# Kernel tuning notes

Hardware: AMD Instinct MI355X
Metric: run time of the kernel (lower is better)

The kernel has to match this reference:

```python
import jax, jax.numpy as jnp
import numpy as np
import math

B, S, D, H = 4, 1024, 1024, 16
HD = D // H  # 64
EPS = 1e-6
LOG2E = 1.442695041


def setup_inputs() -> dict:
    key = jax.random.key(0)
    ks = jax.random.split(key, 8)
    inputs_q = jax.random.normal(ks[0], (B, S, D), dtype=jnp.float32)
    patch_mask = jnp.zeros((B, S), dtype=bool)
    w_scale = 0.02
    Wq = jax.random.normal(ks[1], (D, D), dtype=jnp.float32) * w_scale
    Wk = jax.random.normal(ks[2], (D, D), dtype=jnp.float32) * w_scale
    Wv = jax.random.normal(ks[3], (D, D), dtype=jnp.float32) * w_scale
    Wo = jax.random.normal(ks[4], (D, D), dtype=jnp.float32) * w_scale
    # RMSNorm scales (torch inits to zero; use random nonzero for a meaningful baseline)
    q_ln_scale = jax.random.uniform(ks[5], (HD,), dtype=jnp.float32, minval=0.5, maxval=1.5)
    k_ln_scale = jax.random.uniform(ks[6], (HD,), dtype=jnp.float32, minval=0.5, maxval=1.5)
    per_dim_scale = jax.random.normal(ks[7], (HD,), dtype=jnp.float32) * 0.1
    return {"inputs_q": inputs_q, "patch_mask": patch_mask, "Wq": Wq, "Wk": Wk,
            "Wv": Wv, "Wo": Wo, "q_ln_scale": q_ln_scale, "k_ln_scale": k_ln_scale,
            "per_dim_scale": per_dim_scale}


def _rope(x, position):
    # x: [b, s, h, hd]; position: [b, s] (float)
    half = HD // 2
    fraction = 2.0 * jnp.arange(half, dtype=x.dtype) / HD
    timescale = 10000.0 ** fraction  # min_timescale=1, max=10000
    sinusoid = position[:, :, None, None] / timescale[None, None, None, :]
    sin, cos = jnp.sin(sinusoid), jnp.cos(sinusoid)
    x1, x2 = jnp.split(x, 2, axis=-1)
    return jnp.concatenate([x1 * cos - x2 * sin, x2 * cos + x1 * sin], axis=-1)


def _rms_norm(x, scale):
    var = jnp.mean(jnp.square(x), axis=-1, keepdims=True)
    return x * jax.lax.rsqrt(var + EPS) * scale


def reference(inputs_q, patch_mask, Wq, Wk, Wv, Wo, q_ln_scale, k_ln_scale, per_dim_scale):
    b, n, _ = inputs_q.shape
    # torch nn.Linear: y = x @ W.T
    q = jnp.einsum('bsd,fd->bsf', inputs_q, Wq).reshape(b, n, H, HD)
    k = jnp.einsum('bsd,fd->bsf', inputs_q, Wk).reshape(b, n, H, HD)
    v = jnp.einsum('bsd,fd->bsf', inputs_q, Wv).reshape(b, n, H, HD)

    num_masked = jnp.sum(patch_mask.astype(jnp.int32), axis=-1, keepdims=True)  # [b,1]
    position = (jnp.arange(n)[None, :] - num_masked).astype(inputs_q.dtype)  # [b,s]

    q = _rope(q, position)
    k = _rope(k, position)
    q = _rms_norm(q, q_ln_scale)
    k = _rms_norm(k, k_ln_scale)
    # per-dim scale (replaces the usual 1/sqrt(d) since SDPA runs with scale=1.0)
    q = q * (LOG2E / math.sqrt(HD) * jax.nn.softplus(per_dim_scale))

    # mask: q_idx >= kv_idx AND kv_idx >= num_masked  -> [b,1,q,kv]
    qi = jnp.arange(n)[None, None, :, None]
    ki = jnp.arange(n)[None, None, None, :]
    attn_mask = (qi >= ki) & (ki >= num_masked[:, None, None])

    scores = jnp.einsum('bqhd,bkhd->bhqk', q, k)  # scale=1.0
    scores = jnp.where(attn_mask, scores, jnp.asarray(-1e30, scores.dtype))
    attn = jax.nn.softmax(scores, axis=-1)
    x = jnp.einsum('bhqk,bkhd->bqhd', attn, v).reshape(b, n, D)
    return jnp.einsum('bsd,fd->bsf', x, Wo)
```

## Files before the change

kernel.cpp:

```cpp
#include <hip/hip_runtime.h>
#include <hip/hip_bf16.h>
#include <stdint.h>

#define B_  4
#define S_  1024
#define D_  1024
#define H_  16
#define HD_ 64

using f32x4  = __attribute__((ext_vector_type(4))) float;
using bf16x8 = __attribute__((ext_vector_type(8))) __bf16;
using bf16x4 = __attribute__((ext_vector_type(4))) __bf16;
using f32x4v = __attribute__((ext_vector_type(4))) float;

__device__ __forceinline__ void g2l16(const void* g, void* l) {
  using gp = const __attribute__((address_space(1))) unsigned int*;
  using lp = __attribute__((address_space(3))) unsigned int*;
  __builtin_amdgcn_global_load_lds((gp)(unsigned long long)g,
                                   (lp)(unsigned int)(unsigned long long)l,
                                   16, 0, 0);
}

__global__ __launch_bounds__(256)
void prep_kernel(const float* __restrict__ X, const float* __restrict__ w0,
                 const float* __restrict__ w1, const float* __restrict__ w2,
                 const float* __restrict__ w3, const unsigned char* __restrict__ mask,
                 const float* __restrict__ qsc, const float* __restrict__ ksc,
                 const float* __restrict__ pds,
                 __bf16* __restrict__ Xb, __bf16* __restrict__ Wqkv,
                 __bf16* __restrict__ Wob, int* __restrict__ nm,
                 float* __restrict__ tab, float* __restrict__ qmul,
                 float* __restrict__ kmul) {
  const int bid = blockIdx.x, tid = threadIdx.x;
  if (bid < 4096) {
    const int i = bid * 1024 + tid * 4;
    f32x4v v = *(const f32x4v*)(X + i);
    bf16x4 o;
    o[0] = (__bf16)v[0]; o[1] = (__bf16)v[1]; o[2] = (__bf16)v[2]; o[3] = (__bf16)v[3];
    *(bf16x4*)(Xb + i) = o;
  } else if (bid < 8192) {
    const int bid2 = bid - 4096;
    const int y = bid2 >> 10;
    const float* src = (y == 0) ? w0 : (y == 1) ? w1 : (y == 2) ? w2 : w3;
    __bf16* dst = (y < 3) ? (Wqkv + (size_t)y * 1048576) : Wob;
    const int i = (bid2 & 1023) * 1024 + tid * 4;
    f32x4v v = *(const f32x4v*)(src + i);
    bf16x4 o;
    o[0] = (__bf16)v[0]; o[1] = (__bf16)v[1]; o[2] = (__bf16)v[2]; o[3] = (__bf16)v[3];
    *(bf16x4*)(dst + i) = o;
  } else if (bid == 8192) {
    const int b = tid >> 6, ln = tid & 63;
    int s = 0;
    for (int i = ln; i < S_; i += 64) s += (mask[b * S_ + i] != 0) ? 1 : 0;
    #pragma unroll
    for (int k = 1; k < 64; k <<= 1) s += __shfl_xor(s, k);
    if (ln == 0) nm[b] = s;
  } else if (bid <= 8321) {
    const int idx = (bid - 8193) * 256 + tid;
    if (idx < 1025 * 32) {
      const int p = idx >> 5, d = idx & 31;
      const float ang = (float)p * exp2f((float)d * -0.41524101186092025f);
      float sn, cs;
      sincosf(ang, &sn, &cs);
      tab[idx * 2]     = sn;
      tab[idx * 2 + 1] = cs;
    }
  } else {
    if (tid < 64) {
      qmul[tid] = qsc[tid] * 0.26017112262570096f * log1pf(expf(pds[tid]));
      kmul[tid] = ksc[tid];
    }
  }
}

template <int MODE>
__global__ __launch_bounds__(256)
void gemm_nt(const __bf16* __restrict__ A, const __bf16* __restrict__ Bm,
             float* __restrict__ Cf, __bf16* __restrict__ Cbf,
             __bf16* __restrict__ Vt, int N, int K) {
  __shared__ __bf16 sA[2][128 * 32];
  __shared__ __bf16 sB[2][128 * 32];
  const int tid = threadIdx.x;
  const int wv = tid >> 6, lane = tid & 63;

  const int nwg = gridDim.x * gridDim.y;
  const int lin = blockIdx.y * gridDim.x + blockIdx.x;
  const int swzid = (lin & 7) * (nwg >> 3) + (lin >> 3);
  const int row0 = (swzid / gridDim.x) * 128;
  const int col0 = (swzid % gridDim.x) * 128;

  const int wm = wv >> 1, wn = wv & 1;
  const int c0 = wv * 2, c1 = c0 + 1;
  const int srow = lane >> 2;
  const int scol = (((lane & 3) ^ ((lane >> 3) & 3))) * 8;
  const __bf16* Ab = A + (size_t)(row0 + srow) * K + scol;
  const __bf16* Bb = Bm + (size_t)(col0 + srow) * K + scol;
  const int fr = lane & 15;
  const int fk = ((lane >> 4) ^ ((fr >> 1) & 3)) * 8;

  f32x4 acc[4][4] = {};

#define GSTAGE(buf, k0) do {                                              \
    g2l16(Ab + (size_t)(c0 * 16) * K + (k0), &sA[buf][c0 * 512]);         \
    g2l16(Ab + (size_t)(c1 * 16) * K + (k0), &sA[buf][c1 * 512]);         \
    g2l16(Bb + (size_t)(c0 * 16) * K + (k0), &sB[buf][c0 * 512]);         \
    g2l16(Bb + (size_t)(c1 * 16) * K + (k0), &sB[buf][c1 * 512]);         \
  } while (0)

  GSTAGE(0, 0);
  __syncthreads();
  int cur = 0;
  for (int k0 = 0; k0 < K; k0 += 32) {
    if (k0 + 32 < K) GSTAGE(cur ^ 1, k0 + 32);

    bf16x8 af[4], bfr[4];
    #pragma unroll
    for (int m = 0; m < 4; ++m)
      af[m] = *(const bf16x8*)&sA[cur][(wm * 64 + m * 16 + fr) * 32 + fk];
    #pragma unroll
    for (int n = 0; n < 4; ++n)
      bfr[n] = *(const bf16x8*)&sB[cur][(wn * 64 + n * 16 + fr) * 32 + fk];

    #pragma unroll
    for (int m = 0; m < 4; ++m)
      #pragma unroll
      for (int n = 0; n < 4; ++n)
        acc[m][n] = __builtin_amdgcn_mfma_f32_16x16x32_bf16(af[m], bfr[n], acc[m][n], 0, 0, 0);

    __syncthreads();
    cur ^= 1;
  }
#undef GSTAGE

  const int g4 = (lane >> 4) * 4;
  if (MODE == 0) {
    #pragma unroll
    for (int m = 0; m < 4; ++m)
      #pragma unroll
      for (int n = 0; n < 4; ++n)
        #pragma unroll
        for (int r = 0; r < 4; ++r)
          Cf[(size_t)(row0 + wm * 64 + m * 16 + g4 + r) * N + col0 + wn * 64 + n * 16 + fr] =
              acc[m][n][r];
    return;
  }

  if (col0 >= 2048) {
    #pragma unroll
    for (int m = 0; m < 4; ++m) {
      const int row = row0 + wm * 64 + m * 16 + g4;
      const int bq = row >> 10, s = row & 1023;
      #pragma unroll
      for (int n = 0; n < 4; ++n) {
        const int hd = col0 + wn * 64 + n * 16 + fr - 2048;
        bf16x4 ov;
        #pragma unroll
        for (int r = 0; r < 4; ++r) ov[r] = (__bf16)acc[m][n][r];
        *(bf16x4*)&Vt[(size_t)((bq * H_ + (hd >> 6)) * HD_ + (hd & 63)) * S_ + s] = ov;
      }
    }
  } else {
    #pragma unroll
    for (int m = 0; m < 4; ++m)
      #pragma unroll
      for (int n = 0; n < 4; ++n)
        #pragma unroll
        for (int r = 0; r < 4; ++r)
          Cbf[(size_t)(row0 + wm * 64 + m * 16 + g4 + r) * N + col0 + wn * 64 + n * 16 + fr] =
              (__bf16)acc[m][n][r];
  }
}

__global__ __launch_bounds__(256)
void rope_rms(const __bf16* __restrict__ QKV, __bf16* __restrict__ Qr,
              __bf16* __restrict__ Kr, const float* __restrict__ qmul,
              const float* __restrict__ kmul, const int* __restrict__ nm,
              const float* __restrict__ tab) {
  const int gt = blockIdx.x * 256 + threadIdx.x;
  const int j = gt & 3;
  const int h = (gt >> 2) & 15;
  const int s = (gt >> 6) & 1023;
  const int b = (gt >> 16) & 3;
  const bool isK = gt >= 262144;
  const int dlo = j * 8;

  const __bf16* src = QKV + (size_t)(b * S_ + s) * 3072 + (isK ? 1024 : 0) + h * HD_ + dlo;
  bf16x8 xl = *(const bf16x8*)src;
  bf16x8 xh = *(const bf16x8*)(src + 32);

  const int ip = s - nm[b];
  const int ap = ip < 0 ? -ip : ip;
  const float sgn = ip < 0 ? -1.f : 1.f;
  const float* trow = tab + (size_t)ap * 64 + dlo * 2;
  f32x4v tv[4];
  #pragma unroll
  for (int k = 0; k < 4; ++k) tv[k] = *(const f32x4v*)(trow + k * 4);

  float ol[8], oh[8];
  float ss = 0.f;
  #pragma unroll
  for (int i = 0; i < 8; ++i) {
    const float fl = (float)xl[i];
    const float fh = (float)xh[i];
    const float sn = sgn * tv[i >> 1][(i & 1) * 2];
    const float cs = tv[i >> 1][(i & 1) * 2 + 1];
    ol[i] = fl * cs - fh * sn;
    oh[i] = fh * cs + fl * sn;
    ss += ol[i] * ol[i] + oh[i] * oh[i];
  }
  ss += __shfl_xor(ss, 1);
  ss += __shfl_xor(ss, 2);
  const float rn = rsqrtf(ss * (1.0f / 64.0f) + 1e-6f);

  const float* mul = isK ? kmul : qmul;
  f32x4v ml0 = *(const f32x4v*)(mul + dlo);
  f32x4v ml1 = *(const f32x4v*)(mul + dlo + 4);
  f32x4v mh0 = *(const f32x4v*)(mul + dlo + 32);
  f32x4v mh1 = *(const f32x4v*)(mul + dlo + 36);

  bf16x8 outl, outh;
  #pragma unroll
  for (int i = 0; i < 4; ++i) {
    outl[i]     = (__bf16)(ol[i] * rn * ml0[i]);
    outl[i + 4] = (__bf16)(ol[i + 4] * rn * ml1[i]);
    outh[i]     = (__bf16)(oh[i] * rn * mh0[i]);
    outh[i + 4] = (__bf16)(oh[i + 4] * rn * mh1[i]);
  }
  __bf16* dst = (isK ? Kr : Qr) + ((size_t)(b * H_ + h) * S_ + s) * HD_ + dlo;
  *(bf16x8*)dst = outl;
  *(bf16x8*)(dst + 32) = outh;
}

__global__ __launch_bounds__(256)
void attn_fwd(const __bf16* __restrict__ Qr, const __bf16* __restrict__ Kr,
              const __bf16* __restrict__ Vt, __bf16* __restrict__ Ob,
              const int* __restrict__ nm) {
  const int bid = blockIdx.x;
  const int qblk = 15 - (bid >> 6);
  const int bh = bid & 63;
  const int b = bh >> 4, h = bh & 15;
  const int q0 = qblk * 64;
  const int tid = threadIdx.x, wv = tid >> 6, lane = tid & 63;

  __shared__ __bf16 sK[2][64 * 64];
  __shared__ __bf16 sV[2][64 * 64];
  __shared__ unsigned int sP[4][16 * 32];

  const size_t bhs = (size_t)(b * H_ + h);
  const __bf16* Qh = Qr + bhs * (S_ * HD_);
  const __bf16* Kh = Kr + bhs * (S_ * HD_);
  const __bf16* Vh = Vt + bhs * (HD_ * S_);

  const int fr = lane & 15, g = lane >> 4;
  const int qbase = q0 + wv * 16;
  const int q = qbase + fr;
  unsigned int* sPw = &sP[wv][0];
  const int swz = (fr & 7) << 2;

  bf16x8 qf[2];
  #pragma unroll
  for (int ks = 0; ks < 2; ++ks)
    qf[ks] = *(const bf16x8*)&Qh[(size_t)q * HD_ + ks * 32 + g * 8];

  f32x4 oacc[4] = {};
  float mrun = -3e38f, lrun = 0.f;

  const int nmb = nm[b];
  const int srow = lane >> 3;
  const int ssw = ((lane & 7) ^ srow) * 8;
  const int c0 = wv * 2, c1 = c0 + 1;

#define ASTAGE(buf, kv) do {                                                    \
    g2l16(&Kh[(size_t)((kv) + c0 * 8 + srow) * HD_ + ssw], &sK[buf][c0 * 512]); \
    g2l16(&Kh[(size_t)((kv) + c1 * 8 + srow) * HD_ + ssw], &sK[buf][c1 * 512]); \
    g2l16(&Vh[(size_t)(c0 * 8 + srow) * S_ + (kv) + ssw], &sV[buf][c0 * 512]);  \
    g2l16(&Vh[(size_t)(c1 * 8 + srow) * S_ + (kv) + ssw], &sV[buf][c1 * 512]);  \
  } while (0)

  ASTAGE(0, 0);
  __syncthreads();
  int cur = 0;
  const int kvend = q0 + 64;

  for (int kv0 = 0; kv0 < kvend; kv0 += 64) {
    if (kv0 + 64 < kvend) ASTAGE(cur ^ 1, kv0 + 64);

    f32x4 sacc[4] = {};
    __builtin_amdgcn_s_setprio(1);
    #pragma unroll
    for (int n = 0; n < 4; ++n) {
      const int krow = n * 16 + fr;
      #pragma unroll
      for (int ks = 0; ks < 2; ++ks) {
        bf16x8 kf = *(const bf16x8*)&sK[cur][krow * 64 + ((ks * 32 + g * 8) ^ ((krow & 7) * 8))];
        sacc[n] = __builtin_amdgcn_mfma_f32_16x16x32_bf16(kf, qf[ks], sacc[n], 0, 0, 0);
      }
    }
    __builtin_amdgcn_s_setprio(0);

    const bool fullv = (qbase >= kv0 + 63) && (kv0 >= nmb);
    if (!fullv) {
      #pragma unroll
      for (int n = 0; n < 4; ++n)
        #pragma unroll
        for (int r = 0; r < 4; ++r) {
          const int kv = kv0 + n * 16 + g * 4 + r;
          if (q < kv || kv < nmb) sacc[n][r] = -1e30f;
        }
    }

    float pmax = sacc[0][0];
    #pragma unroll
    for (int n = 0; n < 4; ++n)
      #pragma unroll
      for (int r = 0; r < 4; ++r) pmax = fmaxf(pmax, sacc[n][r]);
    pmax = fmaxf(pmax, __shfl_xor(pmax, 16));
    pmax = fmaxf(pmax, __shfl_xor(pmax, 32));
    if (pmax > mrun + 8.f) {
      const float scl = exp2f(mrun - pmax);
      lrun *= scl;
      #pragma unroll
      for (int nd = 0; nd < 4; ++nd)
        #pragma unroll
        for (int r = 0; r < 4; ++r) oacc[nd][r] *= scl;
      mrun = pmax;
    }
    float ls = 0.f;
    #pragma unroll
    for (int n = 0; n < 4; ++n)
      #pragma unroll
      for (int r = 0; r < 4; ++r) {
        const float p = exp2f(sacc[n][r] - mrun);
        sacc[n][r] = p;
        ls += p;
      }
    ls += __shfl_xor(ls, 16);
    ls += __shfl_xor(ls, 32);
    lrun += ls;

    #pragma unroll
    for (int n = 0; n < 4; ++n) {
      union { unsigned int u; __bf16 hh[2]; } p0, p1;
      p0.hh[0] = (__bf16)sacc[n][0]; p0.hh[1] = (__bf16)sacc[n][1];
      p1.hh[0] = (__bf16)sacc[n][2]; p1.hh[1] = (__bf16)sacc[n][3];
      const unsigned long long pu =
          (unsigned long long)p0.u | ((unsigned long long)p1.u << 32);
      *(unsigned long long*)&sPw[fr * 32 + ((n * 8 + g * 2) ^ swz)] = pu;
    }
    bf16x8 pf[2];
    #pragma unroll
    for (int ks = 0; ks < 2; ++ks)
      pf[ks] = *(const bf16x8*)&sPw[fr * 32 + ((ks * 16 + g * 4) ^ swz)];

    __builtin_amdgcn_s_setprio(1);
    #pragma unroll
    for (int nd = 0; nd < 4; ++nd) {
      const int vrow = nd * 16 + fr;
      #pragma unroll
      for (int ks = 0; ks < 2; ++ks) {
        bf16x8 vf = *(const bf16x8*)&sV[cur][vrow * 64 + ((ks * 32 + g * 8) ^ ((vrow & 7) * 8))];
        oacc[nd] = __builtin_amdgcn_mfma_f32_16x16x32_bf16(vf, pf[ks], oacc[nd], 0, 0, 0);
      }
    }
    __builtin_amdgcn_s_setprio(0);

    __syncthreads();
    cur ^= 1;
  }
#undef ASTAGE

  const float inv = 1.0f / lrun;
  __bf16* orow = Ob + (size_t)(b * S_ + q) * D_ + h * HD_;
  #pragma unroll
  for (int nd = 0; nd < 4; ++nd) {
    bf16x4 ov;
    #pragma unroll
    for (int r = 0; r < 4; ++r) ov[r] = (__bf16)(oacc[nd][r] * inv);
    *(bf16x4*)&orow[nd * 16 + g * 4] = ov;
  }
}

extern "C" void kernel_launch(void* const* d_in, const int* in_sizes, int n_in,
                              void* d_out, int out_size, void* d_ws, size_t ws_size,
                              hipStream_t stream) {
  (void)in_sizes; (void)n_in; (void)out_size; (void)ws_size;
  const float* X  = (const float*)d_in[0];
  const unsigned char* pm = (const unsigned char*)d_in[1];
  const float* Wq = (const float*)d_in[2];
  const float* Wk = (const float*)d_in[3];
  const float* Wv = (const float*)d_in[4];
  const float* Wo = (const float*)d_in[5];
  const float* qs = (const float*)d_in[6];
  const float* ks = (const float*)d_in[7];
  const float* pd = (const float*)d_in[8];
  float* out = (float*)d_out;

  char* ws = (char*)d_ws;
  int*    nm   = (int*)ws;
  __bf16* Wqkv = (__bf16*)(ws + 256);
  __bf16* Wob  = (__bf16*)(ws + 256 + 6291456);
  __bf16* Xb   = (__bf16*)(ws + 8388864);
  __bf16* QKV  = (__bf16*)(ws + 16777472);
  __bf16* Krb  = (__bf16*)(ws + 41943296);
  __bf16* Vtb  = (__bf16*)(ws + 50331904);
  float*  tab  = (float*)(ws + 58720512);
  float*  qmul = (float*)(ws + 58982912);
  float*  kmul = (float*)(ws + 58983168);
  __bf16* Qrb  = Xb;
  __bf16* Obuf = QKV;

  prep_kernel<<<8323, 256, 0, stream>>>(X, Wq, Wk, Wv, Wo, pm, qs, ks, pd,
                                        Xb, Wqkv, Wob, nm, tab, qmul, kmul);

  gemm_nt<1><<<dim3(24, 32), 256, 0, stream>>>(Xb, Wqkv, nullptr, QKV, Vtb, 3072, 1024);

  rope_rms<<<2048, 256, 0, stream>>>(QKV, Qrb, Krb, qmul, kmul, nm, tab);

  attn_fwd<<<1024, 256, 0, stream>>>(Qrb, Krb, Vtb, Obuf, nm);

  gemm_nt<0><<<dim3(8, 32), 256, 0, stream>>>(Obuf, Wob, out, nullptr, nullptr, 1024, 1024);
}
```

Baseline: 102.4 us.

## Deepen GEMM LDS pipeline to two stages ahead with explicit waitcnt barriers

Restructures the projection GEMM main loop to prefetch two k-tiles ahead into the double buffer. Fragments are read into registers before a barrier, so the buffer just consumed can be refilled while the MFMAs run. Explicit vmcnt/lgkmcnt waits and raw s_barrier replace __syncthreads, and s_setprio raises priority around the MFMA block. This aims to hide global-load latency better, at the cost of fragile hand-tuned wait counts that rely on the fixed number of global_load_lds issued per stage.

```diff
diff --git a/kernel.cpp b/kernel.cpp
--- a/kernel.cpp
+++ b/kernel.cpp
@@ -108,10 +108,14 @@
   } while (0)
 
   GSTAGE(0, 0);
-  __syncthreads();
-  int cur = 0;
-  for (int k0 = 0; k0 < K; k0 += 32) {
-    if (k0 + 32 < K) GSTAGE(cur ^ 1, k0 + 32);
+  GSTAGE(1, 32);
+  asm volatile("s_waitcnt vmcnt(4)" ::: "memory");
+  __builtin_amdgcn_sched_barrier(0);
+  __builtin_amdgcn_s_barrier();
+
+  const int NT = K >> 5;
+  for (int T = 0; T < NT; ++T) {
+    const int cur = T & 1;
 
     bf16x8 af[4], bfr[4];
     #pragma unroll
@@ -120,15 +124,35 @@
     #pragma unroll
     for (int n = 0; n < 4; ++n)
       bfr[n] = *(const bf16x8*)&sB[cur][(wn * 64 + n * 16 + fr) * 32 + fk];
-
-    #pragma unroll
-    for (int m = 0; m < 4; ++m)
-      #pragma unroll
-      for (int n = 0; n < 4; ++n)
-        acc[m][n] = __builtin_amdgcn_mfma_f32_16x16x32_bf16(af[m], bfr[n], acc[m][n], 0, 0, 0);
-
-    __syncthreads();
-    cur ^= 1;
+    asm volatile("s_waitcnt lgkmcnt(0)" ::: "memory");
+    __builtin_amdgcn_sched_barrier(0);
+    __builtin_amdgcn_s_barrier();
+
+    if (T + 2 < NT) {
+      GSTAGE(cur, (T + 2) * 32);
+
+      __builtin_amdgcn_s_setprio(1);
+      #pragma unroll
+      for (int m = 0; m < 4; ++m)
+        #pragma unroll
+        for (int n = 0; n < 4; ++n)
+          acc[m][n] = __builtin_amdgcn_mfma_f32_16x16x32_bf16(af[m], bfr[n], acc[m][n], 0, 0, 0);
+      __builtin_amdgcn_s_setprio(0);
+
+      asm volatile("s_waitcnt vmcnt(4)" ::: "memory");
+    } else {
+      __builtin_amdgcn_s_setprio(1);
+      #pragma unroll
+      for (int m = 0; m < 4; ++m)
+        #pragma unroll
+        for (int n = 0; n < 4; ++n)
+          acc[m][n] = __builtin_amdgcn_mfma_f32_16x16x32_bf16(af[m], bfr[n], acc[m][n], 0, 0, 0);
+      __builtin_amdgcn_s_setprio(0);
+
+      asm volatile("s_waitcnt vmcnt(0)" ::: "memory");
+    }
+    __builtin_amdgcn_sched_barrier(0);
+    __builtin_amdgcn_s_barrier();
   }
 #undef GSTAGE
 
```

Result: slower. 125.3 us (+22.3%).
